# Optimization experiments

Hardware: AMD Instinct MI355X
Metric: run time of the kernel (lower is better)

## Reference

```python
import jax, jax.numpy as jnp
import numpy as np

B, T, E, H = 4, 2048, 1024, 16
D = E // H

def setup_inputs() -> dict:
    key = jax.random.key(0)
    ks = jax.random.split(key, 8)
    s = 0.02
    return {
        "q": jax.random.normal(ks[0], (B, T, E), dtype=jnp.float32),
        "k": jax.random.normal(ks[1], (B, T, E), dtype=jnp.float32),
        "v": jax.random.normal(ks[2], (B, T, E), dtype=jnp.float32),
        "Wq": jax.random.normal(ks[3], (E, E), dtype=jnp.float32) * s,
        "Wk": jax.random.normal(ks[4], (E, E), dtype=jnp.float32) * s,
        "Wv": jax.random.normal(ks[5], (E, E), dtype=jnp.float32) * s,
        "Wp": jax.random.normal(ks[6], (E, E), dtype=jnp.float32) * s,
        "bp": jnp.zeros((E,), dtype=jnp.float32),
    }

def reference(q, k, v, Wq, Wk, Wv, Wp, bp):
    # Linear projections (torch Linear: x @ W.T). NOTE: original code computes
    # key from the already-projected query (k = self.key(q)); external k is unused.
    qp = q @ Wq.T                      # [B,T,E]
    kp = qp @ Wk.T                     # [B,T,E]  <- faithful quirk
    vp = v @ Wv.T                      # [B,T,E]
    qh = qp.reshape(B, T, H, D).transpose(0, 2, 1, 3)  # [B,H,T,D]
    kh = kp.reshape(B, T, H, D).transpose(0, 2, 1, 3)
    vh = vp.reshape(B, T, H, D).transpose(0, 2, 1, 3)
    # Faithful quirk: att = scores / D**(-1/2) == scores * sqrt(D)
    scale = jnp.float32(D) ** 0.5
    att = jnp.einsum('bhtd,bhsd->bhts', qh, kh) * scale  # [B,H,T,T]
    causal = jnp.tril(jnp.ones((T, T), dtype=bool))
    att = jnp.where(causal, att, -jnp.inf)
    att = jax.nn.softmax(att, axis=-1)
    y = jnp.einsum('bhts,bhsd->bhtd', att, vh)           # [B,H,T,D]
    y = y.transpose(0, 2, 1, 3).reshape(B, T, E)
    return y @ Wp.T + bp
```

## Files before the change

kernel.cpp:

```cpp
#include <hip/hip_runtime.h>


typedef unsigned short u16;
typedef unsigned int   u32;
typedef __attribute__((ext_vector_type(8))) __bf16 bf16x8;
typedef __attribute__((ext_vector_type(8))) u16    u16x8;
typedef __attribute__((ext_vector_type(4))) u16    u16x4;
typedef __attribute__((ext_vector_type(4))) float  f32x4;
typedef __attribute__((ext_vector_type(4))) int    i32x4;

#define DEV static __device__ __forceinline__

DEV u16 f2bf(float x){ union{float f;u32 u;}v; v.f=x; u32 r=v.u+0x7fffu+((v.u>>16)&1u); return (u16)(r>>16); }
DEV float bf2f(u16 b){ union{u32 u;float f;}v; v.u=((u32)b)<<16; return v.f; }
DEV f32x4 zero4(){ f32x4 z={0.f,0.f,0.f,0.f}; return z; }
DEV f32x4 mfma16(bf16x8 a, bf16x8 b, f32x4 c){ return __builtin_amdgcn_mfma_f32_16x16x32_bf16(a,b,c,0,0,0); }
DEV void gld16(const u16* g, u16* l){
  __builtin_amdgcn_global_load_lds((const __attribute__((address_space(1))) u32*)g,
                                   (__attribute__((address_space(3))) u32*)l, 16, 0, 0);
}
DEV u32 pkbf(float a, float b){
  union{float f;u32 u;}x,y; x.f=a; y.f=b;
  return __builtin_amdgcn_perm(y.u+0x8000u, x.u+0x8000u, 0x07060302u);
}

constexpr int B_=4, T_=2048, E_=1024;
constexpr int M_=B_*T_;
constexpr float L2E8 = 11.5415603f;

__global__ __launch_bounds__(256)
void cvt_a(const float* __restrict__ q, const float* __restrict__ v,
           u16* __restrict__ qi, u16* __restrict__ vb)
{
  const int j=blockIdx.y;
  const size_t e=((size_t)blockIdx.x*256+threadIdx.x)*8;
  const float* s=(j==0)?q:v;
  f32x4 x0=*reinterpret_cast<const f32x4*>(s+e);
  f32x4 x1=*reinterpret_cast<const f32x4*>(s+e+4);
  u16x8 h,l;
#pragma unroll
  for(int t=0;t<4;t++){
    u16 hh=f2bf(x0[t]); h[t]=hh; l[t]=f2bf(x0[t]-bf2f(hh));
    u16 h2=f2bf(x1[t]); h[t+4]=h2; l[t+4]=f2bf(x1[t]-bf2f(h2));
  }
  if(j==0){
    const size_t row=e>>10, k=e&1023;
    u16* d=qi + row*2048 + (k>>3)*16;
    *reinterpret_cast<u16x8*>(d)=h;
    *reinterpret_cast<u16x8*>(d+8)=l;
  } else {
    *reinterpret_cast<u16x8*>(vb+e)=h;
  }
}

__global__ __launch_bounds__(256)
void cvt_w(const float* __restrict__ Wq, const float* __restrict__ Wk, const float* __restrict__ Wv,
           u16* __restrict__ wqi, u16* __restrict__ wki, u16* __restrict__ wvb)
{
  const int j=blockIdx.y;
  const size_t e=((size_t)blockIdx.x*256+threadIdx.x)*8;
  const float* s=(j==0)?Wq:(j==1)?Wk:Wv;
  f32x4 x0=*reinterpret_cast<const f32x4*>(s+e);
  f32x4 x1=*reinterpret_cast<const f32x4*>(s+e+4);
  u16x8 h,l;
#pragma unroll
  for(int t=0;t<4;t++){
    u16 hh=f2bf(x0[t]); h[t]=hh; l[t]=f2bf(x0[t]-bf2f(hh));
    u16 h2=f2bf(x1[t]); h[t+4]=h2; l[t+4]=f2bf(x1[t]-bf2f(h2));
  }
  if(j==2){ *reinterpret_cast<u16x8*>(wvb+e)=h; return; }
  u16* base=(j==0)?wqi:wki;
  const size_t row=e>>10, k=e&1023;
  u16* d=base + row*2048 + (k>>3)*16;
  *reinterpret_cast<u16x8*>(d)=h;
  *reinterpret_cast<u16x8*>(d+8)=l;
}

__global__ __launch_bounds__(256)
void cvt_p(const float* __restrict__ Wp, u16* __restrict__ wpb)
{
  const size_t e=((size_t)blockIdx.x*256+threadIdx.x)*8;
  f32x4 x0=*reinterpret_cast<const f32x4*>(Wp+e);
  f32x4 x1=*reinterpret_cast<const f32x4*>(Wp+e+4);
  u16x8 h;
#pragma unroll
  for(int t=0;t<4;t++){ h[t]=f2bf(x0[t]); h[t+4]=f2bf(x1[t]); }
  *reinterpret_cast<u16x8*>(wpb+e)=h;
}

template<int SPLIT,int OMODE>
__global__ __launch_bounds__(256)
void gemm(const u16* __restrict__ Ag, const u16* __restrict__ Bg,
          const float* __restrict__ bias,
          u16* __restrict__ Ob, float* __restrict__ Of, int ldc)
{
  __shared__ u16 sA[SPLIT?128*128:128*64];
  __shared__ u16 sB[SPLIT?128*128:128*64];

  const int tid=threadIdx.x, wave=tid>>6, lane=tid&63;
  const int quad=lane>>4, l16=lane&15, sw=l16&7;
  const int wm=(wave>>1)*64, wn=(wave&1)*64;
  const int n0=blockIdx.x*128, m0=blockIdx.y*128;

  f32x4 acc[4][4];
#pragma unroll
  for(int i=0;i<4;i++)
#pragma unroll
    for(int j=0;j<4;j++) acc[i][j]=zero4();

  for(int k0=0;k0<E_;k0+=64){
    if(SPLIT){
#pragma unroll
      for(int it=0;it<8;it++){
        const int c=it*256+tid, row=c>>4, j=(c&15)^(row&7);
        gld16(Ag + (size_t)(m0+row)*2048 + k0*2 + j*8, &sA[(it*256+wave*64)*8]);
      }
#pragma unroll
      for(int it=0;it<8;it++){
        const int c=it*256+tid, row=c>>4, j=(c&15)^(row&7);
        gld16(Bg + (size_t)(n0+row)*2048 + k0*2 + j*8, &sB[(it*256+wave*64)*8]);
      }
    } else {
#pragma unroll
      for(int it=0;it<4;it++){
        const int c=it*256+tid, row=c>>3, j=(c&7)^(row&7);
        gld16(Ag + (size_t)(m0+row)*1024 + k0 + j*8, &sA[(it*256+wave*64)*8]);
      }
#pragma unroll
      for(int it=0;it<4;it++){
        const int c=it*256+tid, row=c>>3, j=(c&7)^(row&7);
        gld16(Bg + (size_t)(n0+row)*1024 + k0 + j*8, &sB[(it*256+wave*64)*8]);
      }
    }
    __syncthreads();

#pragma unroll
    for(int kk=0;kk<2;kk++){
      if(SPLIT){
        bf16x8 ahh[4],ahl[4],bhh[4],bhl[4];
#pragma unroll
        for(int i=0;i<4;i++){
          const u16* pa=&sA[(wm+i*16+l16)*128];
          const u16* pb=&sB[(wn+i*16+l16)*128];
          const int ch=2*(kk*4+quad);
          ahh[i]=*reinterpret_cast<const bf16x8*>(&pa[((ch  )^sw)*8]);
          ahl[i]=*reinterpret_cast<const bf16x8*>(&pa[((ch+1)^sw)*8]);
          bhh[i]=*reinterpret_cast<const bf16x8*>(&pb[((ch  )^sw)*8]);
          bhl[i]=*reinterpret_cast<const bf16x8*>(&pb[((ch+1)^sw)*8]);
        }
#pragma unroll
        for(int i=0;i<4;i++)
#pragma unroll
          for(int j=0;j<4;j++){
            acc[i][j]=mfma16(ahh[i],bhh[j],acc[i][j]);
            acc[i][j]=mfma16(ahh[i],bhl[j],acc[i][j]);
            acc[i][j]=mfma16(ahl[i],bhh[j],acc[i][j]);
          }
      } else {
        bf16x8 a[4],b[4];
#pragma unroll
        for(int i=0;i<4;i++){
          a[i]=*reinterpret_cast<const bf16x8*>(&sA[(wm+i*16+l16)*64 + (((kk*4+quad)^sw)*8)]);
          b[i]=*reinterpret_cast<const bf16x8*>(&sB[(wn+i*16+l16)*64 + (((kk*4+quad)^sw)*8)]);
        }
#pragma unroll
        for(int i=0;i<4;i++)
#pragma unroll
          for(int j=0;j<4;j++)
            acc[i][j]=mfma16(a[i],b[j],acc[i][j]);
      }
    }
    __syncthreads();
  }

#pragma unroll
  for(int i=0;i<4;i++)
#pragma unroll
    for(int j=0;j<4;j++){
      const int col=n0+wn+j*16+l16;
#pragma unroll
      for(int r=0;r<4;r++){
        const int row=m0+wm+i*16+quad*4+r;
        float v=acc[i][j][r];
        if(OMODE==2)      Of[(size_t)row*ldc+col]=v+bias[col];
        else if(OMODE==1) Ob[(size_t)row*ldc+col]=f2bf(v);
        else {
          u16 hh=f2bf(v);
          const size_t base=(size_t)row*2048 + (size_t)(col>>3)*16 + (col&7);
          Ob[base]=hh; Ob[base+8]=f2bf(v-bf2f(hh));
        }
      }
    }
}

__global__ __launch_bounds__(256)
void attn(const u16* __restrict__ qpi, const u16* __restrict__ kpi,
          const u16* __restrict__ vpT, u16* __restrict__ yout)
{
  __shared__ u16 sK [64*128];
  __shared__ u16 sVT[64*64];

  const int tid=threadIdx.x, wave=tid>>6, lane=tid&63;
  const int quad=lane>>4, l16=lane&15, sw=l16&7;
  const int qt=(int)(gridDim.x-1-blockIdx.x)>>6;
  const int bh=blockIdx.x&63;
  const int b=bh>>4, h=bh&15;
  const int qr0=qt*128+wave*32;

  bf16x8 qfh[2][2], qfl[2][2];
#pragma unroll
  for(int mt=0;mt<2;mt++)
#pragma unroll
    for(int ksv=0;ksv<2;ksv++){
      const size_t off=(size_t)(b*T_+qr0+mt*16+l16)*2048 + h*128 + (ksv*4+quad)*16;
      qfh[mt][ksv]=*reinterpret_cast<const bf16x8*>(qpi+off);
      qfl[mt][ksv]=*reinterpret_cast<const bf16x8*>(qpi+off+8);
    }

  float mst[2]={-1e30f,-1e30f}, lst[2]={0.f,0.f};
  f32x4 oacc[2][4];
#pragma unroll
  for(int mt=0;mt<2;mt++)
#pragma unroll
    for(int dt=0;dt<4;dt++) oacc[mt][dt]=zero4();

  const int nkt=2*(qt+1);
  for(int kt=0;kt<nkt;kt++){
    const int s0=kt*64;
    __syncthreads();
#pragma unroll
    for(int it=0;it<4;it++){
      const int c=it*256+tid, row=c>>4, j=(c&15)^(row&7);
      gld16(kpi + (size_t)(b*T_+s0+row)*2048 + h*128 + j*8,
            &sK[(it*256+wave*64)*8]);
    }
#pragma unroll
    for(int it=0;it<2;it++){
      const int c=it*256+tid, row=c>>3, j=(c&7)^(row&7);
      gld16(vpT + (size_t)(h*64+row)*8192 + b*T_ + s0 + j*8,
            &sVT[(it*256+wave*64)*8]);
    }
    __syncthreads();

    if(s0<=qr0+31){
      f32x4 sacc[4][2];
#pragma unroll
      for(int st=0;st<4;st++)
#pragma unroll
        for(int mt=0;mt<2;mt++) sacc[st][mt]=zero4();
#pragma unroll
      for(int st=0;st<4;st++)
#pragma unroll
        for(int ksv=0;ksv<2;ksv++){
          const u16* pk=&sK[(st*16+l16)*128];
          const int ch=2*(ksv*4+quad);
          bf16x8 kh=*reinterpret_cast<const bf16x8*>(&pk[((ch  )^sw)*8]);
          bf16x8 kl=*reinterpret_cast<const bf16x8*>(&pk[((ch+1)^sw)*8]);
#pragma unroll
          for(int mt=0;mt<2;mt++){
            sacc[st][mt]=mfma16(kh,qfh[mt][ksv],sacc[st][mt]);
            sacc[st][mt]=mfma16(kl,qfh[mt][ksv],sacc[st][mt]);
            sacc[st][mt]=mfma16(kh,qfl[mt][ksv],sacc[st][mt]);
          }
        }
      const bool needmask=(s0+63>qr0);
      u32 pk_[4][2][2];
#pragma unroll
      for(int mt=0;mt<2;mt++){
        const int qrow=qr0+mt*16+l16;
        float mloc=-1e30f;
#pragma unroll
        for(int st=0;st<4;st++)
#pragma unroll
          for(int r=0;r<4;r++){
            float v=sacc[st][mt][r];
            if(needmask && (s0+st*16+quad*4+r>qrow)) v=-1e30f;
            sacc[st][mt][r]=v;
            mloc=fmaxf(mloc,v);
          }
        mloc=fmaxf(mloc,__shfl_xor(mloc,16,64));
        mloc=fmaxf(mloc,__shfl_xor(mloc,32,64));
        const float nm=fmaxf(mst[mt],mloc);
        const float alpha=exp2f((mst[mt]-nm)*L2E8);
        mst[mt]=nm;
        const float cexp=nm*L2E8;
        float rs=0.f;
#pragma unroll
        for(int st=0;st<4;st++)
#pragma unroll
          for(int r=0;r<4;r++){
            float p=exp2f(__builtin_fmaf(sacc[st][mt][r],L2E8,-cexp));
            sacc[st][mt][r]=p;
            rs+=p;
          }
        lst[mt]=lst[mt]*alpha+rs;
#pragma unroll
        for(int dt=0;dt<4;dt++) oacc[mt][dt]*=alpha;
#pragma unroll
        for(int st=0;st<4;st++){
          pk_[st][mt][0]=pkbf(sacc[st][mt][0],sacc[st][mt][1]);
          pk_[st][mt][1]=pkbf(sacc[st][mt][2],sacc[st][mt][3]);
        }
      }
      const int srcA=(2*(quad&1))*16+l16, srcB=srcA+16;
      const bool hs=(quad>=2);
#pragma unroll
      for(int ksv=0;ksv<2;ksv++){
        bf16x8 b2[2];
#pragma unroll
        for(int mt=0;mt<2;mt++){
          int e0=__shfl((int)pk_[2*ksv  ][mt][0],srcA,64);
          int g0=__shfl((int)pk_[2*ksv+1][mt][0],srcA,64);
          int e1=__shfl((int)pk_[2*ksv  ][mt][1],srcA,64);
          int g1=__shfl((int)pk_[2*ksv+1][mt][1],srcA,64);
          int e2=__shfl((int)pk_[2*ksv  ][mt][0],srcB,64);
          int g2=__shfl((int)pk_[2*ksv+1][mt][0],srcB,64);
          int e3=__shfl((int)pk_[2*ksv  ][mt][1],srcB,64);
          int g3=__shfl((int)pk_[2*ksv+1][mt][1],srcB,64);
          i32x4 bd={ hs?g0:e0, hs?g1:e1, hs?g2:e2, hs?g3:e3 };
          b2[mt]=*reinterpret_cast<bf16x8*>(&bd);
        }
#pragma unroll
        for(int dt=0;dt<4;dt++){
          bf16x8 va=*reinterpret_cast<const bf16x8*>(&sVT[(dt*16+l16)*64 + (((ksv*4+quad)^sw)*8)]);
#pragma unroll
          for(int mt=0;mt<2;mt++)
            oacc[mt][dt]=mfma16(va,b2[mt],oacc[mt][dt]);
        }
      }
    }
  }
#pragma unroll
  for(int mt=0;mt<2;mt++){
    float lt=lst[mt];
    lt+=__shfl_xor(lt,16,64);
    lt+=__shfl_xor(lt,32,64);
    const float inv=1.0f/lt;
    const size_t rb=(size_t)(b*T_+qr0+mt*16+l16)*1024 + h*64;
#pragma unroll
    for(int dt=0;dt<4;dt++){
      u16x4 o4;
#pragma unroll
      for(int r=0;r<4;r++) o4[r]=f2bf(oacc[mt][dt][r]*inv);
      *reinterpret_cast<u16x4*>(yout + rb + dt*16 + quad*4)=o4;
    }
  }
}

extern "C" void kernel_launch(void* const* d_in, const int* in_sizes, int n_in,
                              void* d_out, int out_size, void* d_ws, size_t ws_size,
                              hipStream_t stream)
{
  const float* q =(const float*)d_in[0];
  const float* v =(const float*)d_in[2];
  const float* Wq=(const float*)d_in[3];
  const float* Wk=(const float*)d_in[4];
  const float* Wv=(const float*)d_in[5];
  const float* Wp=(const float*)d_in[6];
  const float* bp=(const float*)d_in[7];
  float* out=(float*)d_out;

  const size_t NE=(size_t)M_*E_;
  const size_t WE=(size_t)E_*E_;
  u16* wsv=(u16*)d_ws;
  u16* qsl_i=wsv;
  u16* qp_i =wsv+2*NE;
  u16* kp_i =wsv;
  u16* wp_b =wsv+2*NE;
  u16* vpT  =wsv+4*NE;
  u16* ybf  =wsv+5*NE;
  u16* og   =(u16*)d_out;
  u16* wq_i =og;
  u16* wk_i =og+2*WE;
  u16* wv_b =og+4*WE;
  u16* vb   =og+5*WE;

  dim3 blk(256);
  cvt_a<<<dim3(NE/2048,2), blk, 0, stream>>>(q, v, qsl_i, vb);
  cvt_w<<<dim3(WE/2048,3), blk, 0, stream>>>(Wq, Wk, Wv, wq_i, wk_i, wv_b);

  dim3 g(E_/128, M_/128);
  gemm<1,0><<<g, blk, 0, stream>>>(qsl_i, wq_i, nullptr, qp_i, nullptr, 0);
  gemm<1,0><<<g, blk, 0, stream>>>(qp_i, wk_i, nullptr, kp_i, nullptr, 0);
  gemm<0,1><<<dim3(M_/128, E_/128), blk, 0, stream>>>(wv_b, vb, nullptr, vpT, nullptr, M_);
  attn<<<dim3(1024), blk, 0, stream>>>(qp_i, kp_i, vpT, ybf);
  cvt_p<<<dim3(WE/2048), blk, 0, stream>>>(Wp, wp_b);
  gemm<0,2><<<g, blk, 0, stream>>>(ybf, wp_b, bp, nullptr, out, E_);
}
```

Baseline: 428.1 us.

## Precompute Wk·Wq product, fuse Q/K projections, shrink GEMM tiles, skip unmasked-tile masking

Computes the combined weight Wk@Wq once via a transposed Wq conversion, so both qp and kp come from the raw q in one GEMM with a doubled N dimension, written to two outputs. This removes the serial dependency of the K projection on the Q projection. Other changes ride along: Wp conversion is folded into cvt_w, GEMM tiles get a smaller K step and narrower N tile with launch_bounds occupancy 4, and attention skips mask checks on fully unmasked tiles. Reassociating the product changes rounding slightly, and the extra 1024^3 weight GEMM adds some work.

```diff
diff --git a/kernel.cpp b/kernel.cpp
--- a/kernel.cpp
+++ b/kernel.cpp
@@ -54,12 +54,14 @@
 }
 
 __global__ __launch_bounds__(256)
-void cvt_w(const float* __restrict__ Wq, const float* __restrict__ Wk, const float* __restrict__ Wv,
-           u16* __restrict__ wqi, u16* __restrict__ wki, u16* __restrict__ wvb)
+void cvt_w(const float* __restrict__ Wq, const float* __restrict__ Wk,
+           const float* __restrict__ Wv, const float* __restrict__ Wp,
+           u16* __restrict__ wqi, u16* __restrict__ wki,
+           u16* __restrict__ wvb, u16* __restrict__ wpb)
 {
   const int j=blockIdx.y;
   const size_t e=((size_t)blockIdx.x*256+threadIdx.x)*8;
-  const float* s=(j==0)?Wq:(j==1)?Wk:Wv;
+  const float* s=(j==0)?Wq:(j==1)?Wk:(j==2)?Wv:Wp;
   f32x4 x0=*reinterpret_cast<const f32x4*>(s+e);
   f32x4 x1=*reinterpret_cast<const f32x4*>(s+e+4);
   u16x8 h,l;
@@ -68,7 +70,7 @@
     u16 hh=f2bf(x0[t]); h[t]=hh; l[t]=f2bf(x0[t]-bf2f(hh));
     u16 h2=f2bf(x1[t]); h[t+4]=h2; l[t+4]=f2bf(x1[t]-bf2f(h2));
   }
-  if(j==2){ *reinterpret_cast<u16x8*>(wvb+e)=h; return; }
+  if(j>=2){ *reinterpret_cast<u16x8*>(((j==2)?wvb:wpb)+e)=h; return; }
   u16* base=(j==0)?wqi:wki;
   const size_t row=e>>10, k=e&1023;
   u16* d=base + row*2048 + (k>>3)*16;
@@ -77,106 +79,116 @@
 }
 
 __global__ __launch_bounds__(256)
-void cvt_p(const float* __restrict__ Wp, u16* __restrict__ wpb)
-{
-  const size_t e=((size_t)blockIdx.x*256+threadIdx.x)*8;
-  f32x4 x0=*reinterpret_cast<const f32x4*>(Wp+e);
-  f32x4 x1=*reinterpret_cast<const f32x4*>(Wp+e+4);
-  u16x8 h;
-#pragma unroll
-  for(int t=0;t<4;t++){ h[t]=f2bf(x0[t]); h[t+4]=f2bf(x1[t]); }
-  *reinterpret_cast<u16x8*>(wpb+e)=h;
-}
-
-template<int SPLIT,int OMODE>
-__global__ __launch_bounds__(256)
+void cvt_t(const float* __restrict__ W, u16* __restrict__ oT)
+{
+  __shared__ float t[64][65];
+  const int r0=blockIdx.y*64, c0=blockIdx.x*64, tid=threadIdx.x;
+#pragma unroll
+  for(int p=0;p<4;p++){
+    const int r=p*16+(tid>>4), c=(tid&15)*4;
+    f32x4 v=*reinterpret_cast<const f32x4*>(W+(size_t)(r0+r)*1024 + c0+c);
+#pragma unroll
+    for(int g=0;g<4;g++) t[r][c+g]=v[g];
+  }
+  __syncthreads();
+  const int cc=tid>>2, ks=(tid&3)*16;
+#pragma unroll
+  for(int g=0;g<2;g++){
+    u16x8 h,l;
+#pragma unroll
+    for(int u=0;u<8;u++){
+      float x=t[ks+g*8+u][cc];
+      u16 hh=f2bf(x); h[u]=hh; l[u]=f2bf(x-bf2f(hh));
+    }
+    u16* d=oT + (size_t)(c0+cc)*2048 + (size_t)((r0+ks)>>3)*16 + g*16;
+    *reinterpret_cast<u16x8*>(d)=h;
+    *reinterpret_cast<u16x8*>(d+8)=l;
+  }
+}
+
+template<int SPLIT,int NT,int OMODE>
+__global__ __launch_bounds__(256,4)
 void gemm(const u16* __restrict__ Ag, const u16* __restrict__ Bg,
           const float* __restrict__ bias,
-          u16* __restrict__ Ob, float* __restrict__ Of, int ldc)
-{
-  __shared__ u16 sA[SPLIT?128*128:128*64];
-  __shared__ u16 sB[SPLIT?128*128:128*64];
+          u16* __restrict__ Ob, u16* __restrict__ Ob2,
+          float* __restrict__ Of, int ldc)
+{
+  constexpr int JN=NT/32;
+  __shared__ u16 sA[128*64];
+  __shared__ u16 sB[NT*64];
 
   const int tid=threadIdx.x, wave=tid>>6, lane=tid&63;
   const int quad=lane>>4, l16=lane&15, sw=l16&7;
-  const int wm=(wave>>1)*64, wn=(wave&1)*64;
-  const int n0=blockIdx.x*128, m0=blockIdx.y*128;
-
-  f32x4 acc[4][4];
+  const int wm=(wave>>1)*64, wn=(wave&1)*(NT/2);
+  const int n0=blockIdx.x*NT, m0=blockIdx.y*128;
+  constexpr int KSTEP=SPLIT?32:64;
+
+  f32x4 acc[4][JN];
 #pragma unroll
   for(int i=0;i<4;i++)
 #pragma unroll
-    for(int j=0;j<4;j++) acc[i][j]=zero4();
-
-  for(int k0=0;k0<E_;k0+=64){
+    for(int j=0;j<JN;j++) acc[i][j]=zero4();
+
+  for(int k0=0;k0<E_;k0+=KSTEP){
+#pragma unroll
+    for(int it=0;it<4;it++){
+      const int c=it*256+tid, row=c>>3, j=(c&7)^(row&7);
+      const u16* ga = SPLIT ? Ag + (size_t)(m0+row)*2048 + (size_t)k0*2 + j*8
+                            : Ag + (size_t)(m0+row)*1024 + k0 + j*8;
+      gld16(ga, &sA[(it*256+wave*64)*8]);
+    }
+#pragma unroll
+    for(int it=0;it<NT/32;it++){
+      const int c=it*256+tid, row=c>>3, j=(c&7)^(row&7);
+      const u16* gb = SPLIT ? Bg + (size_t)(n0+row)*2048 + (size_t)k0*2 + j*8
+                            : Bg + (size_t)(n0+row)*1024 + k0 + j*8;
+      gld16(gb, &sB[(it*256+wave*64)*8]);
+    }
+    __syncthreads();
+
     if(SPLIT){
-#pragma unroll
-      for(int it=0;it<8;it++){
-        const int c=it*256+tid, row=c>>4, j=(c&15)^(row&7);
-        gld16(Ag + (size_t)(m0+row)*2048 + k0*2 + j*8, &sA[(it*256+wave*64)*8]);
-      }
-#pragma unroll
-      for(int it=0;it<8;it++){
-        const int c=it*256+tid, row=c>>4, j=(c&15)^(row&7);
-        gld16(Bg + (size_t)(n0+row)*2048 + k0*2 + j*8, &sB[(it*256+wave*64)*8]);
+      bf16x8 ahh[4],ahl[4];
+#pragma unroll
+      for(int i=0;i<4;i++){
+        const u16* pa=&sA[(wm+i*16+l16)*64];
+        ahh[i]=*reinterpret_cast<const bf16x8*>(&pa[((2*quad  )^sw)*8]);
+        ahl[i]=*reinterpret_cast<const bf16x8*>(&pa[((2*quad+1)^sw)*8]);
+      }
+#pragma unroll
+      for(int j=0;j<JN;j++){
+        const u16* pb=&sB[(wn+j*16+l16)*64];
+        bf16x8 bhh=*reinterpret_cast<const bf16x8*>(&pb[((2*quad  )^sw)*8]);
+        bf16x8 bhl=*reinterpret_cast<const bf16x8*>(&pb[((2*quad+1)^sw)*8]);
+#pragma unroll
+        for(int i=0;i<4;i++){
+          acc[i][j]=mfma16(ahh[i],bhh,acc[i][j]);
+          acc[i][j]=mfma16(ahh[i],bhl,acc[i][j]);
+          acc[i][j]=mfma16(ahl[i],bhh,acc[i][j]);
+        }
       }
     } else {
 #pragma unroll
-      for(int it=0;it<4;it++){
-        const int c=it*256+tid, row=c>>3, j=(c&7)^(row&7);
-        gld16(Ag + (size_t)(m0+row)*1024 + k0 + j*8, &sA[(it*256+wave*64)*8]);
-      }
-#pragma unroll
-      for(int it=0;it<4;it++){
-        const int c=it*256+tid, row=c>>3, j=(c&7)^(row&7);
-        gld16(Bg + (size_t)(n0+row)*1024 + k0 + j*8, &sB[(it*256+wave*64)*8]);
+      for(int kk=0;kk<2;kk++){
+        bf16x8 a[4];
+#pragma unroll
+        for(int i=0;i<4;i++)
+          a[i]=*reinterpret_cast<const bf16x8*>(&sA[(wm+i*16+l16)*64 + (((kk*4+quad)^sw)*8)]);
+#pragma unroll
+        for(int j=0;j<JN;j++){
+          bf16x8 b=*reinterpret_cast<const bf16x8*>(&sB[(wn+j*16+l16)*64 + (((kk*4+quad)^sw)*8)]);
+#pragma unroll
+          for(int i=0;i<4;i++)
+            acc[i][j]=mfma16(a[i],b,acc[i][j]);
+        }
       }
     }
     __syncthreads();
-
-#pragma unroll
-    for(int kk=0;kk<2;kk++){
-      if(SPLIT){
-        bf16x8 ahh[4],ahl[4],bhh[4],bhl[4];
-#pragma unroll
-        for(int i=0;i<4;i++){
-          const u16* pa=&sA[(wm+i*16+l16)*128];
-          const u16* pb=&sB[(wn+i*16+l16)*128];
-          const int ch=2*(kk*4+quad);
-          ahh[i]=*reinterpret_cast<const bf16x8*>(&pa[((ch  )^sw)*8]);
-          ahl[i]=*reinterpret_cast<const bf16x8*>(&pa[((ch+1)^sw)*8]);
-          bhh[i]=*reinterpret_cast<const bf16x8*>(&pb[((ch  )^sw)*8]);
-          bhl[i]=*reinterpret_cast<const bf16x8*>(&pb[((ch+1)^sw)*8]);
-        }
-#pragma unroll
-        for(int i=0;i<4;i++)
-#pragma unroll
-          for(int j=0;j<4;j++){
-            acc[i][j]=mfma16(ahh[i],bhh[j],acc[i][j]);
-            acc[i][j]=mfma16(ahh[i],bhl[j],acc[i][j]);
-            acc[i][j]=mfma16(ahl[i],bhh[j],acc[i][j]);
-          }
-      } else {
-        bf16x8 a[4],b[4];
-#pragma unroll
-        for(int i=0;i<4;i++){
-          a[i]=*reinterpret_cast<const bf16x8*>(&sA[(wm+i*16+l16)*64 + (((kk*4+quad)^sw)*8)]);
-          b[i]=*reinterpret_cast<const bf16x8*>(&sB[(wn+i*16+l16)*64 + (((kk*4+quad)^sw)*8)]);
-        }
-#pragma unroll
-        for(int i=0;i<4;i++)
-#pragma unroll
-          for(int j=0;j<4;j++)
-            acc[i][j]=mfma16(a[i],b[j],acc[i][j]);
-      }
-    }
-    __syncthreads();
   }
 
 #pragma unroll
   for(int i=0;i<4;i++)
 #pragma unroll
-    for(int j=0;j<4;j++){
+    for(int j=0;j<JN;j++){
       const int col=n0+wn+j*16+l16;
 #pragma unroll
       for(int r=0;r<4;r++){
@@ -185,9 +197,11 @@
         if(OMODE==2)      Of[(size_t)row*ldc+col]=v+bias[col];
         else if(OMODE==1) Ob[(size_t)row*ldc+col]=f2bf(v);
         else {
+          u16* base=(col<1024)?Ob:Ob2;
+          const int c1=col&1023;
+          const size_t ba=(size_t)row*2048 + (size_t)(c1>>3)*16 + (c1&7);
           u16 hh=f2bf(v);
-          const size_t base=(size_t)row*2048 + (size_t)(col>>3)*16 + (col&7);
-          Ob[base]=hh; Ob[base+8]=f2bf(v-bf2f(hh));
+          base[ba]=hh; base[ba+8]=f2bf(v-bf2f(hh));
         }
       }
     }
@@ -269,15 +283,22 @@
       for(int mt=0;mt<2;mt++){
         const int qrow=qr0+mt*16+l16;
         float mloc=-1e30f;
-#pragma unroll
-        for(int st=0;st<4;st++)
-#pragma unroll
-          for(int r=0;r<4;r++){
-            float v=sacc[st][mt][r];
-            if(needmask && (s0+st*16+quad*4+r>qrow)) v=-1e30f;
-            sacc[st][mt][r]=v;
-            mloc=fmaxf(mloc,v);
-          }
+        if(needmask){
+#pragma unroll
+          for(int st=0;st<4;st++)
+#pragma unroll
+            for(int r=0;r<4;r++){
+              float v=sacc[st][mt][r];
+              if(s0+st*16+quad*4+r>qrow) v=-1e30f;
+              sacc[st][mt][r]=v;
+              mloc=fmaxf(mloc,v);
+            }
+        } else {
+#pragma unroll
+          for(int st=0;st<4;st++)
+#pragma unroll
+            for(int r=0;r<4;r++) mloc=fmaxf(mloc,sacc[st][mt][r]);
+        }
         mloc=fmaxf(mloc,__shfl_xor(mloc,16,64));
         mloc=fmaxf(mloc,__shfl_xor(mloc,32,64));
         const float nm=fmaxf(mst[mt],mloc);
@@ -363,27 +384,27 @@
   const size_t NE=(size_t)M_*E_;
   const size_t WE=(size_t)E_*E_;
   u16* wsv=(u16*)d_ws;
-  u16* qsl_i=wsv;
-  u16* qp_i =wsv+2*NE;
-  u16* kp_i =wsv;
-  u16* wp_b =wsv+2*NE;
-  u16* vpT  =wsv+4*NE;
-  u16* ybf  =wsv+5*NE;
+  u16* wq_i =wsv;
+  u16* wqk_i=wsv+2*WE;
+  u16* wk_i =wsv+4*WE;
+  u16* wv_b =wsv+6*WE;
+  u16* wp_b =wsv+7*WE;
+  u16* vb   =wsv+8*WE;
+  u16* ybf  =vb;
+  u16* qp_i =wsv+8*WE+NE;
+  u16* kp_i =wsv+8*WE+3*NE;
+  u16* wqT_i=kp_i;
   u16* og   =(u16*)d_out;
-  u16* wq_i =og;
-  u16* wk_i =og+2*WE;
-  u16* wv_b =og+4*WE;
-  u16* vb   =og+5*WE;
+  u16* qs_i =og;
+  u16* vpT  =og;
 
   dim3 blk(256);
-  cvt_a<<<dim3(NE/2048,2), blk, 0, stream>>>(q, v, qsl_i, vb);
-  cvt_w<<<dim3(WE/2048,3), blk, 0, stream>>>(Wq, Wk, Wv, wq_i, wk_i, wv_b);
-
-  dim3 g(E_/128, M_/128);
-  gemm<1,0><<<g, blk, 0, stream>>>(qsl_i, wq_i, nullptr, qp_i, nullptr, 0);
-  gemm<1,0><<<g, blk, 0, stream>>>(qp_i, wk_i, nullptr, kp_i, nullptr, 0);
-  gemm<0,1><<<dim3(M_/128, E_/128), blk, 0, stream>>>(wv_b, vb, nullptr, vpT, nullptr, M_);
+  cvt_a<<<dim3(NE/2048,2), blk, 0, stream>>>(q, v, qs_i, vb);
+  cvt_w<<<dim3(WE/2048,4), blk, 0, stream>>>(Wq, Wk, Wv, Wp, wq_i, wk_i, wv_b, wp_b);
+  cvt_t<<<dim3(16,16), blk, 0, stream>>>(Wq, wqT_i);
+  gemm<1,128,0><<<dim3(8,8), blk, 0, stream>>>(wk_i, wqT_i, nullptr, wqk_i, wqk_i, nullptr, 0);
+  gemm<1,128,0><<<dim3(16,64), blk, 0, stream>>>(qs_i, wq_i, nullptr, qp_i, kp_i, nullptr, 0);
+  gemm<0,64,1><<<dim3(128,8), blk, 0, stream>>>(wv_b, vb, nullptr, vpT, nullptr, nullptr, M_);
   attn<<<dim3(1024), blk, 0, stream>>>(qp_i, kp_i, vpT, ybf);
-  cvt_p<<<dim3(WE/2048), blk, 0, stream>>>(Wp, wp_b);
-  gemm<0,2><<<g, blk, 0, stream>>>(ybf, wp_b, bp, nullptr, out, E_);
-}
+  gemm<0,64,2><<<dim3(16,64), blk, 0, stream>>>(ybf, wp_b, bp, nullptr, nullptr, out, E_);
+}
```

New measurement: 481.9 us. 1.13x slower.
